# Kernel optimization log

Hardware: AMD Instinct MI355X
Metric: run time of the kernel (lower is better)

## Reference

```python
import jax, jax.numpy as jnp
import numpy as np

T, B, I, H = 2048, 64, 256, 256

def setup_inputs() -> dict:
    key = jax.random.key(0)
    k_x, k_wih, k_whh = jax.random.split(key, 3)
    x = jax.random.normal(k_x, (T, B, I), dtype=jnp.float32)
    h0 = jnp.zeros((1, B, H), dtype=jnp.float32)
    # nn.RNN weight_ih_l0 init: U(-1/sqrt(H), 1/sqrt(H)); shape [H, I]
    bound = 1.0 / np.sqrt(H)
    W_ih = jax.random.uniform(k_wih, (H, I), minval=-bound, maxval=bound, dtype=jnp.float32)
    # IndRNN recurrent weight: diagonal vector, U(-1, 1); biases are zeroed.
    w_hh = jax.random.uniform(k_whh, (H,), minval=-1.0, maxval=1.0, dtype=jnp.float32)
    return {"x": x, "h0": h0, "W_ih": W_ih, "w_hh": w_hh}

def reference(x, h0, W_ih, w_hh):
    # Precompute the input projection for all timesteps (the only GEMM):
    # [T, B, H] = x @ W_ih^T  (biases are zero)
    xW = jnp.einsum('tbi,hi->tbh', x, W_ih)

    def step(h, xw_t):
        # IndRNN: diagonal recurrence -> elementwise multiply instead of matmul
        h_new = jax.nn.relu(xw_t + h * w_hh)
        return h_new, h_new

    h_last, outputs = jax.lax.scan(step, h0[0], xW)
    return outputs, h_last[None]  # ([T,B,H], [1,B,H]) matching nn.RNN
```

## Files before the change

kernel.cpp:

```cpp
#include <hip/hip_runtime.h>

typedef short v8s __attribute__((ext_vector_type(8)));
typedef float v4f __attribute__((ext_vector_type(4)));

#define BH 16384
#define TBH 33554432
#define SEG 16
#define SEGT 128
#define SCAN_TILE 128
#define NTILE 16

__device__ __forceinline__ ushort f2bf(float f) {
  uint u = __float_as_uint(f);
  u += 0x7FFF + ((u >> 16) & 1);
  return (ushort)(u >> 16);
}

__device__ __forceinline__ uint pkbf2(float a, float b) {
  uint r;
  asm("v_cvt_pk_bf16_f32 %0, %1, %2" : "=v"(r) : "v"(a), "v"(b));
  return r;
}

union frag_u { uint u[4]; v8s s; };

__global__ __launch_bounds__(256) void indrnn_w2bf(
    const float* __restrict__ W, ushort* __restrict__ Wbf)
{
  const int g   = blockIdx.x * 256 + threadIdx.x;
  const int kc  = g >> 11;
  const int rem = g & 2047;
  const int row = rem >> 3;
  const int sp  = rem & 7;
  const int slog = sp ^ (row & 7);
  const float* src = W + row * 256 + kc * 64 + slog * 8;
  const float4 f0 = *(const float4*)src;
  const float4 f1 = *(const float4*)(src + 4);
  uint4 o;
  o.x = pkbf2(f0.x, f0.y); o.y = pkbf2(f0.z, f0.w);
  o.z = pkbf2(f1.x, f1.y); o.w = pkbf2(f1.z, f1.w);
  *(uint4*)(Wbf + (size_t)g * 8) = o;
}

__global__ __launch_bounds__(256, 3) void indrnn_gemm(
    const float* __restrict__ A,
    const ushort* __restrict__ Wbf,
    ushort* __restrict__ C)
{
  __shared__ __align__(16) float  Af[4096];
  __shared__ __align__(16) ushort Bs[16384];

  const int tid   = threadIdx.x;
  const int lane  = tid & 63;
  const int wn    = tid >> 6;
  const int l15   = lane & 15;
  const int lhi   = lane >> 4;
  const int m0    = blockIdx.x * 64;
  const int bflat = tid & 192;

  v4f acc[4][4] = {};

  for (int kc = 0; kc < 4; ++kc) {
    if (kc) __syncthreads();

    #pragma unroll
    for (int j = 0; j < 4; ++j) {
      const int bf_ = j * 256 + bflat;
      const int fl  = bf_ + lane;
      const int row = fl >> 4;
      const int sl  = fl & 15;
      const float* src = A + ((size_t)(m0 + row) << 8) + kc * 64 + ((sl ^ (row & 7)) << 2);
      __builtin_amdgcn_global_load_lds(src, &Af[bf_ << 2], 16, 0, 0);
    }
    #pragma unroll
    for (int j = 0; j < 8; ++j) {
      const int bf_ = j * 256 + bflat;
      const int fl  = bf_ + lane;
      __builtin_amdgcn_global_load_lds(
          (const float*)(Wbf + (size_t)kc * 16384 + (size_t)fl * 8),
          (float*)(Bs + (size_t)bf_ * 8), 16, 0, 0);
    }
    asm volatile("s_waitcnt vmcnt(0)" ::: "memory");
    __syncthreads();

    #pragma unroll
    for (int kk = 0; kk < 2; ++kk) {
      v8s bfr[4];
      #pragma unroll
      for (int nt = 0; nt < 4; ++nt) {
        const int row = wn * 64 + nt * 16 + l15;
        const int sp  = (kk * 4 + lhi) ^ (row & 7);
        bfr[nt] = *(const v8s*)((const char*)Bs + row * 128 + sp * 16);
      }
      #pragma unroll
      for (int mt = 0; mt < 4; ++mt) {
        const int row = mt * 16 + l15;
        const int s0  = kk * 8 + lhi * 2;
        const char* base = (const char*)Af + row * 256;
        const float4 lo = *(const float4*)(base + ((s0 ^ (row & 7)) << 4));
        const float4 hi = *(const float4*)(base + (((s0 + 1) ^ (row & 7)) << 4));
        frag_u t;
        t.u[0] = pkbf2(lo.x, lo.y); t.u[1] = pkbf2(lo.z, lo.w);
        t.u[2] = pkbf2(hi.x, hi.y); t.u[3] = pkbf2(hi.z, hi.w);
        #pragma unroll
        for (int nt = 0; nt < 4; ++nt)
          acc[mt][nt] = __builtin_amdgcn_mfma_f32_16x16x32_bf16(t.s, bfr[nt], acc[mt][nt], 0, 0, 0);
      }
    }
  }

  #pragma unroll
  for (int mt = 0; mt < 4; ++mt) {
    #pragma unroll
    for (int nt = 0; nt < 4; ++nt) {
      #pragma unroll
      for (int r = 0; r < 4; ++r) {
        int row = m0 + mt * 16 + lhi * 4 + r;
        int col = wn * 64 + nt * 16 + l15;
        C[((size_t)row << 8) + col] = f2bf(acc[mt][nt][r]);
      }
    }
  }
}

__global__ __launch_bounds__(256) void indrnn_seg(
    const ushort* __restrict__ xw,
    const float* __restrict__ w_hh,
    float4* __restrict__ fn)
{
  const int chgrp = blockIdx.x & 63;
  const int seg   = blockIdx.x >> 6;
  const int ch    = chgrp * 256 + threadIdx.x;
  const float w   = w_hh[ch & 255];
  const ushort* px = xw + (size_t)seg * SEGT * BH + ch;

  float p = 1.0f, a = 0.0f, lo = -3.402823466e38f, hi = 3.402823466e38f;

  uint b0[16], b1[16];
  auto ldb = [&](uint (&buf)[16], int kb) {
    const ushort* q = px + (size_t)kb * 16 * BH;
    #pragma unroll
    for (int j = 0; j < 16; ++j) buf[j] = q[(size_t)j * BH];
  };
  auto comp = [&](uint (&buf)[16]) {
    #pragma unroll
    for (int j = 0; j < 16; ++j) {
      float xv = __uint_as_float(buf[j] << 16);
      float A = fmaf(w, lo, xv);
      float B = fmaf(w, hi, xv);
      lo = fmaxf(0.0f, fminf(A, B));
      hi = fmaxf(0.0f, fmaxf(A, B));
      a  = fmaf(w, a, xv);
      p *= w;
    }
  };

  ldb(b0, 0); ldb(b1, 1);
  for (int kb = 0; kb < 8; kb += 2) {
    comp(b0); if (kb + 2 < 8) ldb(b0, kb + 2);
    comp(b1); if (kb + 3 < 8) ldb(b1, kb + 3);
  }
  fn[(size_t)seg * BH + ch] = make_float4(p, a, lo, hi);
}

__global__ __launch_bounds__(256) void indrnn_fix(
    const ushort* __restrict__ xw,
    const float* __restrict__ h0,
    const float* __restrict__ w_hh,
    const float4* __restrict__ fn,
    float* __restrict__ out)
{
  const int chgrp = blockIdx.x & 63;
  const int seg   = blockIdx.x >> 6;
  const int ch    = chgrp * 256 + threadIdx.x;
  const float w   = w_hh[ch & 255];

  float h = h0[ch];
  for (int s = 0; s < seg; ++s) {
    const float4 F = fn[(size_t)s * BH + ch];
    h = fminf(fmaxf(fmaf(F.x, h, F.y), F.z), F.w);
  }

  const ushort* px = xw + (size_t)seg * SEGT * BH + ch;
  float*        po = out + (size_t)seg * SEGT * BH + ch;

  uint b0[16], b1[16];
  auto ldb = [&](uint (&buf)[16], int kb) {
    const ushort* q = px + (size_t)kb * 16 * BH;
    #pragma unroll
    for (int j = 0; j < 16; ++j) buf[j] = q[(size_t)j * BH];
  };
  auto cp = [&](uint (&buf)[16], int kb) {
    float* o = po + (size_t)kb * 16 * BH;
    #pragma unroll
    for (int j = 0; j < 16; ++j) {
      float xv = __uint_as_float(buf[j] << 16);
      h = fmaxf(fmaf(h, w, xv), 0.0f);
      o[(size_t)j * BH] = h;
    }
  };

  ldb(b0, 0); ldb(b1, 1);
  for (int kb = 0; kb < 8; kb += 2) {
    cp(b0, kb);     if (kb + 2 < 8) ldb(b0, kb + 2);
    cp(b1, kb + 1); if (kb + 3 < 8) ldb(b1, kb + 3);
  }

  if (seg == SEG - 1) out[(size_t)TBH + ch] = h;
}

__global__ __launch_bounds__(512) void indrnn_gemm_fb(
    const float* __restrict__ A,
    const float* __restrict__ W,
    ushort* __restrict__ C)
{
  __shared__ ushort As[128 * 72];
  __shared__ ushort Bs[256 * 72];

  const int tid  = threadIdx.x;
  const int lane = tid & 63;
  const int wid  = tid >> 6;
  const int wm   = wid >> 2;
  const int wn   = wid & 3;
  const int m0   = blockIdx.x * 128;
  const int l15 = lane & 15;
  const int lhi = lane >> 4;

  v4f acc[4][4] = {};

  for (int kc = 0; kc < 4; ++kc) {
    #pragma unroll
    for (int j = 0; j < 4; ++j) {
      int f    = j * 512 + tid;
      int row  = f >> 4;
      int colf = f & 15;
      const float4 a4 = *(const float4*)(A + ((size_t)(m0 + row) << 8) + kc * 64 + colf * 4);
      ushort4 b4 = make_ushort4(f2bf(a4.x), f2bf(a4.y), f2bf(a4.z), f2bf(a4.w));
      *(ushort4*)(As + row * 72 + colf * 4) = b4;
    }
    #pragma unroll
    for (int j = 0; j < 8; ++j) {
      int f    = j * 512 + tid;
      int row  = f >> 4;
      int colf = f & 15;
      const float4 a4 = *(const float4*)(W + ((size_t)row << 8) + kc * 64 + colf * 4);
      ushort4 b4 = make_ushort4(f2bf(a4.x), f2bf(a4.y), f2bf(a4.z), f2bf(a4.w));
      *(ushort4*)(Bs + row * 72 + colf * 4) = b4;
    }
    __syncthreads();

    #pragma unroll
    for (int kk = 0; kk < 2; ++kk) {
      const int koff = kk * 32 + lhi * 8;
      v8s af[4], bf[4];
      #pragma unroll
      for (int mt = 0; mt < 4; ++mt)
        af[mt] = *(const v8s*)(As + (wm * 64 + mt * 16 + l15) * 72 + koff);
      #pragma unroll
      for (int nt = 0; nt < 4; ++nt)
        bf[nt] = *(const v8s*)(Bs + (wn * 64 + nt * 16 + l15) * 72 + koff);
      #pragma unroll
      for (int mt = 0; mt < 4; ++mt)
        #pragma unroll
        for (int nt = 0; nt < 4; ++nt)
          acc[mt][nt] = __builtin_amdgcn_mfma_f32_16x16x32_bf16(af[mt], bf[nt], acc[mt][nt], 0, 0, 0);
    }
    __syncthreads();
  }

  #pragma unroll
  for (int mt = 0; mt < 4; ++mt)
    #pragma unroll
    for (int nt = 0; nt < 4; ++nt)
      #pragma unroll
      for (int r = 0; r < 4; ++r) {
        int row = m0 + wm * 64 + mt * 16 + lhi * 4 + r;
        int col = wn * 64 + nt * 16 + l15;
        C[((size_t)row << 8) + col] = f2bf(acc[mt][nt][r]);
      }
}

__global__ __launch_bounds__(128) void indrnn_scan(
    const ushort* __restrict__ xw,
    const float* __restrict__ h0,
    const float* __restrict__ w_hh,
    float* __restrict__ out)
{
  __shared__ __align__(16) ushort tile[3][SCAN_TILE * 64];

  const int lane = threadIdx.x & 63;
  const int wv   = threadIdx.x >> 6;
  const int ch0  = blockIdx.x * 64;
  const int ch   = ch0 + lane;

  const size_t psrc0 = (size_t)(lane >> 3) * BH + (size_t)ch0 + ((lane & 7) << 3);

  auto stage = [&](int ti) {
    const ushort* src = xw + (size_t)ti * SCAN_TILE * BH + psrc0;
    ushort* dst = &tile[ti % 3][0];
    #pragma unroll
    for (int j = 0; j < 16; ++j) {
      __builtin_amdgcn_global_load_lds(
          (const float*)(src + (size_t)j * 8 * BH),
          (float*)(dst + j * 512), 16, 0, 0);
    }
  };

  float h = 0.0f, w = 0.0f;
  if (wv == 0) {
    h = h0[ch];
    w = w_hh[ch & 255];
  } else {
    stage(0);
    stage(1);
    asm volatile("s_waitcnt vmcnt(16)" ::: "memory");
  }
  asm volatile("" ::: "memory");
  __builtin_amdgcn_s_barrier();
  __builtin_amdgcn_sched_barrier(0);

  for (int i = 0; i < NTILE; ++i) {
    if (wv == 0) {
      const ushort* tp = &tile[i % 3][lane];
      float* po = out + (size_t)i * SCAN_TILE * BH + ch;
      #pragma unroll
      for (int t = 0; t < SCAN_TILE; t += 16) {
        ushort v[16];
        #pragma unroll
        for (int j = 0; j < 16; ++j) v[j] = tp[(t + j) * 64];
        #pragma unroll
        for (int j = 0; j < 16; ++j) {
          float xv = __uint_as_float((uint)v[j] << 16);
          h = fmaxf(fmaf(h, w, xv), 0.0f);
          po[(size_t)(t + j) * BH] = h;
        }
      }
    } else {
      if (i + 2 < NTILE) {
        stage(i + 2);
        asm volatile("s_waitcnt vmcnt(16)" ::: "memory");
      } else {
        asm volatile("s_waitcnt vmcnt(0)" ::: "memory");
      }
    }
    asm volatile("" ::: "memory");
    __builtin_amdgcn_s_barrier();
    __builtin_amdgcn_sched_barrier(0);
  }

  if (wv == 0) out[(size_t)TBH + ch] = h;
}

extern "C" void kernel_launch(void* const* d_in, const int* in_sizes, int n_in,
                              void* d_out, int out_size, void* d_ws, size_t ws_size,
                              hipStream_t stream) {
  const float* x    = (const float*)d_in[0];
  const float* h0   = (const float*)d_in[1];
  const float* W_ih = (const float*)d_in[2];
  const float* w_hh = (const float*)d_in[3];
  float* out = (float*)d_out;
  ushort* xw = (ushort*)d_ws;

  const size_t off_fn = 64ull << 20;
  const size_t off_wb = off_fn + (size_t)SEG * BH * sizeof(float4);
  const size_t need   = off_wb + 131072;

  if (ws_size >= need) {
    float4* fn  = (float4*)((char*)d_ws + off_fn);
    ushort* wbf = (ushort*)((char*)d_ws + off_wb);
    indrnn_w2bf<<<dim3(32),   dim3(256), 0, stream>>>(W_ih, wbf);
    indrnn_gemm<<<dim3(2048), dim3(256), 0, stream>>>(x, wbf, xw);
    indrnn_seg <<<dim3(1024), dim3(256), 0, stream>>>(xw, w_hh, fn);
    indrnn_fix <<<dim3(1024), dim3(256), 0, stream>>>(xw, h0, w_hh, fn, out);
  } else {
    indrnn_gemm_fb<<<dim3(1024), dim3(512), 0, stream>>>(x, W_ih, xw);
    indrnn_scan<<<dim3(256), dim3(128), 0, stream>>>(xw, h0, w_hh, out);
  }
}
```

Measured before the change: 281.2 us.

## Double-buffer GEMM K-chunks to overlap global-to-LDS loads with MFMA

```diff
diff --git a/kernel.cpp b/kernel.cpp
--- a/kernel.cpp
+++ b/kernel.cpp
@@ -28,12 +28,12 @@
     const float* __restrict__ W, ushort* __restrict__ Wbf)
 {
   const int g   = blockIdx.x * 256 + threadIdx.x;
-  const int kc  = g >> 11;
-  const int rem = g & 2047;
-  const int row = rem >> 3;
-  const int sp  = rem & 7;
-  const int slog = sp ^ (row & 7);
-  const float* src = W + row * 256 + kc * 64 + slog * 8;
+  const int c   = g >> 10;
+  const int rem = g & 1023;
+  const int row = rem >> 2;
+  const int sp  = rem & 3;
+  const int s   = sp ^ ((row >> 1) & 3);
+  const float* src = W + row * 256 + c * 32 + s * 8;
   const float4 f0 = *(const float4*)src;
   const float4 f1 = *(const float4*)(src + 4);
   uint4 o;
@@ -47,66 +47,82 @@
     const ushort* __restrict__ Wbf,
     ushort* __restrict__ C)
 {
-  __shared__ __align__(16) float  Af[4096];
-  __shared__ __align__(16) ushort Bs[16384];
-
-  const int tid   = threadIdx.x;
-  const int lane  = tid & 63;
-  const int wn    = tid >> 6;
-  const int l15   = lane & 15;
-  const int lhi   = lane >> 4;
-  const int m0    = blockIdx.x * 64;
-  const int bflat = tid & 192;
-
-  v4f acc[4][4] = {};
-
-  for (int kc = 0; kc < 4; ++kc) {
-    if (kc) __syncthreads();
-
+  __shared__ __align__(16) float  Af[2][2048];
+  __shared__ __align__(16) ushort Bs[2][8192];
+
+  const int tid  = threadIdx.x;
+  const int lane = tid & 63;
+  const int wn   = tid >> 6;
+  const int l15  = lane & 15;
+  const int lhi  = lane >> 4;
+  const int m0   = blockIdx.x * 64;
+  const int bfl  = tid & 192;
+
+  auto stageA = [&](int c, int buf) {
+    #pragma unroll
+    for (int j = 0; j < 2; ++j) {
+      const int bf_ = j * 256 + bfl;
+      const int fl  = bf_ + lane;
+      const int row = fl >> 3;
+      const int sl  = fl & 7;
+      const float* src = A + ((size_t)(m0 + row) << 8) + c * 32 + ((sl ^ (row & 7)) << 2);
+      __builtin_amdgcn_global_load_lds(src, &Af[buf][bf_ << 2], 16, 0, 0);
+    }
+  };
+  auto stageW = [&](int c, int buf) {
     #pragma unroll
     for (int j = 0; j < 4; ++j) {
-      const int bf_ = j * 256 + bflat;
-      const int fl  = bf_ + lane;
-      const int row = fl >> 4;
-      const int sl  = fl & 15;
-      const float* src = A + ((size_t)(m0 + row) << 8) + kc * 64 + ((sl ^ (row & 7)) << 2);
-      __builtin_amdgcn_global_load_lds(src, &Af[bf_ << 2], 16, 0, 0);
-    }
-    #pragma unroll
-    for (int j = 0; j < 8; ++j) {
-      const int bf_ = j * 256 + bflat;
+      const int bf_ = j * 256 + bfl;
       const int fl  = bf_ + lane;
       __builtin_amdgcn_global_load_lds(
-          (const float*)(Wbf + (size_t)kc * 16384 + (size_t)fl * 8),
-          (float*)(Bs + (size_t)bf_ * 8), 16, 0, 0);
-    }
-    asm volatile("s_waitcnt vmcnt(0)" ::: "memory");
-    __syncthreads();
-
-    #pragma unroll
-    for (int kk = 0; kk < 2; ++kk) {
-      v8s bfr[4];
-      #pragma unroll
-      for (int nt = 0; nt < 4; ++nt) {
-        const int row = wn * 64 + nt * 16 + l15;
-        const int sp  = (kk * 4 + lhi) ^ (row & 7);
-        bfr[nt] = *(const v8s*)((const char*)Bs + row * 128 + sp * 16);
-      }
-      #pragma unroll
-      for (int mt = 0; mt < 4; ++mt) {
-        const int row = mt * 16 + l15;
-        const int s0  = kk * 8 + lhi * 2;
-        const char* base = (const char*)Af + row * 256;
-        const float4 lo = *(const float4*)(base + ((s0 ^ (row & 7)) << 4));
-        const float4 hi = *(const float4*)(base + (((s0 + 1) ^ (row & 7)) << 4));
-        frag_u t;
-        t.u[0] = pkbf2(lo.x, lo.y); t.u[1] = pkbf2(lo.z, lo.w);
-        t.u[2] = pkbf2(hi.x, hi.y); t.u[3] = pkbf2(hi.z, hi.w);
-        #pragma unroll
-        for (int nt = 0; nt < 4; ++nt)
-          acc[mt][nt] = __builtin_amdgcn_mfma_f32_16x16x32_bf16(t.s, bfr[nt], acc[mt][nt], 0, 0, 0);
-      }
-    }
+          (const float*)(Wbf + (size_t)c * 8192 + (size_t)fl * 8),
+          (float*)(&Bs[buf][bf_ * 8]), 16, 0, 0);
+    }
+  };
+
+  v4f acc[4][4] = {};
+
+  stageA(0, 0); stageW(0, 0);
+
+  auto step = [&](int c, int buf) {
+    if (c + 1 < 8) {
+      stageA(c + 1, buf ^ 1);
+      stageW(c + 1, buf ^ 1);
+      asm volatile("s_waitcnt vmcnt(6)" ::: "memory");
+    } else {
+      asm volatile("s_waitcnt vmcnt(0)" ::: "memory");
+    }
+    __builtin_amdgcn_s_barrier();
+    __builtin_amdgcn_sched_barrier(0);
+
+    v8s bfr[4];
+    #pragma unroll
+    for (int nt = 0; nt < 4; ++nt) {
+      const int row = wn * 64 + nt * 16 + l15;
+      const int sp  = lhi ^ ((row >> 1) & 3);
+      bfr[nt] = *(const v8s*)(&Bs[buf][row * 32 + sp * 8]);
+    }
+    #pragma unroll
+    for (int mt = 0; mt < 4; ++mt) {
+      const int row = mt * 16 + l15;
+      const int p0  = (2 * lhi) ^ (row & 7);
+      const int p1  = (2 * lhi + 1) ^ (row & 7);
+      const float4 lo = *(const float4*)(&Af[buf][row * 32 + p0 * 4]);
+      const float4 hi = *(const float4*)(&Af[buf][row * 32 + p1 * 4]);
+      frag_u t;
+      t.u[0] = pkbf2(lo.x, lo.y); t.u[1] = pkbf2(lo.z, lo.w);
+      t.u[2] = pkbf2(hi.x, hi.y); t.u[3] = pkbf2(hi.z, hi.w);
+      #pragma unroll
+      for (int nt = 0; nt < 4; ++nt)
+        acc[mt][nt] = __builtin_amdgcn_mfma_f32_16x16x32_bf16(t.s, bfr[nt], acc[mt][nt], 0, 0, 0);
+    }
+    __builtin_amdgcn_sched_barrier(0);
+    __builtin_amdgcn_s_barrier();
+  };
+
+  for (int cc = 0; cc < 8; cc += 2) {
+    step(cc,     0);
+    step(cc + 1, 1);
   }
 
   #pragma unroll
```

New measurement: 284.3 us. No clear change (+1.1%).

## Halve scan segment length, process two channels per thread, preload whole segment

Applied to the files above, without the earlier changes.

```diff
diff --git a/kernel.cpp b/kernel.cpp
--- a/kernel.cpp
+++ b/kernel.cpp
@@ -5,8 +5,8 @@
 
 #define BH 16384
 #define TBH 33554432
-#define SEG 16
-#define SEGT 128
+#define SEG2 32
+#define SEGT2 64
 #define SCAN_TILE 128
 #define NTILE 16
 
@@ -123,90 +123,83 @@
   }
 }
 
-__global__ __launch_bounds__(256) void indrnn_seg(
+__global__ __launch_bounds__(256, 4) void indrnn_seg(
     const ushort* __restrict__ xw,
     const float* __restrict__ w_hh,
     float4* __restrict__ fn)
 {
-  const int chgrp = blockIdx.x & 63;
-  const int seg   = blockIdx.x >> 6;
-  const int ch    = chgrp * 256 + threadIdx.x;
-  const float w   = w_hh[ch & 255];
-  const ushort* px = xw + (size_t)seg * SEGT * BH + ch;
-
-  float p = 1.0f, a = 0.0f, lo = -3.402823466e38f, hi = 3.402823466e38f;
-
-  uint b0[16], b1[16];
-  auto ldb = [&](uint (&buf)[16], int kb) {
-    const ushort* q = px + (size_t)kb * 16 * BH;
-    #pragma unroll
-    for (int j = 0; j < 16; ++j) buf[j] = q[(size_t)j * BH];
-  };
-  auto comp = [&](uint (&buf)[16]) {
-    #pragma unroll
-    for (int j = 0; j < 16; ++j) {
-      float xv = __uint_as_float(buf[j] << 16);
-      float A = fmaf(w, lo, xv);
-      float B = fmaf(w, hi, xv);
-      lo = fmaxf(0.0f, fminf(A, B));
-      hi = fmaxf(0.0f, fmaxf(A, B));
-      a  = fmaf(w, a, xv);
-      p *= w;
-    }
-  };
-
-  ldb(b0, 0); ldb(b1, 1);
-  for (int kb = 0; kb < 8; kb += 2) {
-    comp(b0); if (kb + 2 < 8) ldb(b0, kb + 2);
-    comp(b1); if (kb + 3 < 8) ldb(b1, kb + 3);
-  }
-  fn[(size_t)seg * BH + ch] = make_float4(p, a, lo, hi);
-}
-
-__global__ __launch_bounds__(256) void indrnn_fix(
+  const int seg = blockIdx.x >> 5;
+  const int cp  = (blockIdx.x & 31) * 256 + threadIdx.x;
+  const int ch  = cp * 2;
+  const float w0 = w_hh[ch & 255];
+  const float w1 = w_hh[(ch + 1) & 255];
+  const ushort* px = xw + (size_t)seg * SEGT2 * BH + ch;
+
+  uint buf[SEGT2];
+  #pragma unroll
+  for (int t = 0; t < SEGT2; ++t)
+    buf[t] = *(const uint*)(px + (size_t)t * BH);
+
+  float p0 = 1.f, a0 = 0.f, lo0 = -3.402823466e38f, hi0 = 3.402823466e38f;
+  float p1 = 1.f, a1 = 0.f, lo1 = -3.402823466e38f, hi1 = 3.402823466e38f;
+  #pragma unroll
+  for (int t = 0; t < SEGT2; ++t) {
+    const float x0 = __uint_as_float(buf[t] << 16);
+    const float x1 = __uint_as_float(buf[t] & 0xFFFF0000u);
+    float A, B;
+    A = fmaf(w0, lo0, x0); B = fmaf(w0, hi0, x0);
+    lo0 = fmaxf(0.f, fminf(A, B)); hi0 = fmaxf(0.f, fmaxf(A, B));
+    a0 = fmaf(w0, a0, x0); p0 *= w0;
+    A = fmaf(w1, lo1, x1); B = fmaf(w1, hi1, x1);
+    lo1 = fmaxf(0.f, fminf(A, B)); hi1 = fmaxf(0.f, fmaxf(A, B));
+    a1 = fmaf(w1, a1, x1); p1 *= w1;
+  }
+  fn[(size_t)seg * BH + ch]     = make_float4(p0, a0, lo0, hi0);
+  fn[(size_t)seg * BH + ch + 1] = make_float4(p1, a1, lo1, hi1);
+}
+
+__global__ __launch_bounds__(256, 4) void indrnn_fix(
     const ushort* __restrict__ xw,
     const float* __restrict__ h0,
     const float* __restrict__ w_hh,
     const float4* __restrict__ fn,
     float* __restrict__ out)
 {
-  const int chgrp = blockIdx.x & 63;
-  const int seg   = blockIdx.x >> 6;
-  const int ch    = chgrp * 256 + threadIdx.x;
-  const float w   = w_hh[ch & 255];
-
-  float h = h0[ch];
+  const int seg = blockIdx.x >> 5;
+  const int cp  = (blockIdx.x & 31) * 256 + threadIdx.x;
+  const int ch  = cp * 2;
+  const float w0 = w_hh[ch & 255];
+  const float w1 = w_hh[(ch + 1) & 255];
+
+  const ushort* px = xw + (size_t)seg * SEGT2 * BH + ch;
+  float*        po = out + (size_t)seg * SEGT2 * BH + ch;
+
+  uint buf[SEGT2];
+  #pragma unroll
+  for (int t = 0; t < SEGT2; ++t)
+    buf[t] = *(const uint*)(px + (size_t)t * BH);
+
+  float h0v = h0[ch], h1v = h0[ch + 1];
   for (int s = 0; s < seg; ++s) {
-    const float4 F = fn[(size_t)s * BH + ch];
-    h = fminf(fmaxf(fmaf(F.x, h, F.y), F.z), F.w);
-  }
-
-  const ushort* px = xw + (size_t)seg * SEGT * BH + ch;
-  float*        po = out + (size_t)seg * SEGT * BH + ch;
-
-  uint b0[16], b1[16];
-  auto ldb = [&](uint (&buf)[16], int kb) {
-    const ushort* q = px + (size_t)kb * 16 * BH;
-    #pragma unroll
-    for (int j = 0; j < 16; ++j) buf[j] = q[(size_t)j * BH];
-  };
-  auto cp = [&](uint (&buf)[16], int kb) {
-    float* o = po + (size_t)kb * 16 * BH;
-    #pragma unroll
-    for (int j = 0; j < 16; ++j) {
-      float xv = __uint_as_float(buf[j] << 16);
-      h = fmaxf(fmaf(h, w, xv), 0.0f);
-      o[(size_t)j * BH] = h;
-    }
-  };
-
-  ldb(b0, 0); ldb(b1, 1);
-  for (int kb = 0; kb < 8; kb += 2) {
-    cp(b0, kb);     if (kb + 2 < 8) ldb(b0, kb + 2);
-    cp(b1, kb + 1); if (kb + 3 < 8) ldb(b1, kb + 3);
-  }
-
-  if (seg == SEG - 1) out[(size_t)TBH + ch] = h;
+    const float4 F0 = fn[(size_t)s * BH + ch];
+    const float4 F1 = fn[(size_t)s * BH + ch + 1];
+    h0v = fminf(fmaxf(fmaf(F0.x, h0v, F0.y), F0.z), F0.w);
+    h1v = fminf(fmaxf(fmaf(F1.x, h1v, F1.y), F1.z), F1.w);
+  }
+
+  #pragma unroll
+  for (int t = 0; t < SEGT2; ++t) {
+    const float x0 = __uint_as_float(buf[t] << 16);
+    const float x1 = __uint_as_float(buf[t] & 0xFFFF0000u);
+    h0v = fmaxf(fmaf(h0v, w0, x0), 0.f);
+    h1v = fmaxf(fmaf(h1v, w1, x1), 0.f);
+    *(float2*)(po + (size_t)t * BH) = make_float2(h0v, h1v);
+  }
+
+  if (seg == SEG2 - 1) {
+    out[(size_t)TBH + ch]     = h0v;
+    out[(size_t)TBH + ch + 1] = h1v;
+  }
 }
 
 __global__ __launch_bounds__(512) void indrnn_gemm_fb(
@@ -362,7 +355,7 @@
   ushort* xw = (ushort*)d_ws;
 
   const size_t off_fn = 64ull << 20;
-  const size_t off_wb = off_fn + (size_t)SEG * BH * sizeof(float4);
+  const size_t off_wb = off_fn + (size_t)SEG2 * BH * sizeof(float4);
   const size_t need   = off_wb + 131072;
 
   if (ws_size >= need) {
```

Measured after the change: 292.2 us. 3.9% more time.
